# Performance work log

Hardware: AMD Instinct MI355X
Metric: run time of the kernel (lower is better)

## Reference

```python
import jax, jax.numpy as jnp
import numpy as np

B, T, S, U = 256, 64, 16, 4  # batch, channels, yt_img_size, upscale_factor


def setup_inputs() -> dict:
    key = jax.random.key(0)
    k1, k2, k3 = jax.random.split(key, 3)
    x = jax.random.normal(k1, (B, T, S, S), dtype=jnp.float32)
    # Stacked per-pixel Linear weights: (P pixels, out=U*U*T, in=T)
    W = jax.random.normal(k2, (S * S, U * U * T, T), dtype=jnp.float32) * 0.05
    b = jax.random.normal(k3, (S * S, U * U * T), dtype=jnp.float32) * 0.01
    return {"x": x, "W": W, "b": b}


def reference(x, W, b):
    Bn, Tn, Sn, _ = x.shape
    P = Sn * Sn
    Un = int(np.sqrt(W.shape[1] // Tn))  # upscale factor, static
    # Per-pixel grouped GEMM: each spatial location has its own Linear(T -> U*U*T)
    xp = x.reshape(Bn, Tn, P).transpose(2, 0, 1)          # (P, B, T)
    y = jnp.einsum('pbt,pot->pbo', xp, W) + b[:, None, :]  # (P, B, U*U*T)
    # Flat output per pixel is viewed as (T, U, U) and scattered to the (i*U:(i+1)*U, j*U:(j+1)*U) patch
    y = y.reshape(Sn, Sn, Bn, Tn, Un, Un)                  # (Si, Sj, B, T, Ui, Uj)
    y = y.transpose(2, 3, 0, 4, 1, 5)                      # (B, T, Si, Ui, Sj, Uj)
    return y.reshape(Bn, Tn, Sn * Un, Sn * Un)
```

## Files before the change

### kernel.cpp

```cpp
#include <hip/hip_runtime.h>
#include <hip/hip_bf16.h>


#define P_PIX 256
#define BATCH 256
#define KDIM 64
#define ODIM 1024
#define LDA 72

using bf16x8 = __attribute__((ext_vector_type(8))) short;
using f32x4  = __attribute__((ext_vector_type(4))) float;

__global__ __launch_bounds__(256) void transpose_convert(
    const float* __restrict__ x, __hip_bfloat16* __restrict__ xp)
{
    __shared__ float tile[64][65];
    const int R = BATCH * KDIM;
    int p0 = (blockIdx.x & 3) * 64;
    int r0 = (blockIdx.x >> 2) * 64;
    int tp = threadIdx.x & 63;
    int t4 = threadIdx.x >> 6;
    #pragma unroll
    for (int i = 0; i < 16; ++i) {
        int r = t4 + i * 4;
        tile[r][tp] = x[(size_t)(r0 + r) * P_PIX + p0 + tp];
    }
    __syncthreads();
    #pragma unroll
    for (int i = 0; i < 16; ++i) {
        int pl = t4 + i * 4;
        xp[(size_t)(p0 + pl) * R + r0 + tp] = __float2bfloat16(tile[tp][pl]);
    }
}

__global__ __launch_bounds__(256, 2) void gemm_pixel(
    const __hip_bfloat16* __restrict__ xp,
    const float* __restrict__ W,
    const float* __restrict__ bias,
    float* __restrict__ out)
{
    __shared__ __hip_bfloat16 As[128 * LDA];
    __shared__ __hip_bfloat16 Bs[128 * LDA];

    int g = blockIdx.x;
    int nt     = g & 7;
    int sjmod4 = (g >> 3) & 3;
    int q      = g >> 5;
    int mt  = q & 1;
    int sjg = (q >> 1) & 3;
    int si  = q >> 3;
    int p  = si * 16 + sjg * 4 + sjmod4;
    int m0 = mt * 128;
    int n0 = nt * 128;
    int tid = threadIdx.x;

    {
        const uint4* src = (const uint4*)(xp + (size_t)p * (BATCH * KDIM) + (size_t)m0 * KDIM);
        #pragma unroll
        for (int c = 0; c < 4; ++c) {
            int idx = c * 256 + tid;
            int row = idx >> 3, ch = idx & 7;
            uint4 v = src[idx];
            *(uint4*)(&As[row * LDA + ch * 8]) = v;
        }
    }
    {
        const float4* src = (const float4*)(W + (size_t)p * (ODIM * KDIM) + (size_t)n0 * KDIM);
        #pragma unroll
        for (int c = 0; c < 8; ++c) {
            int idx = c * 256 + tid;
            int row = idx >> 4, ch = idx & 15;
            float4 v = src[idx];
            __hip_bfloat16 h[4];
            h[0] = __float2bfloat16(v.x); h[1] = __float2bfloat16(v.y);
            h[2] = __float2bfloat16(v.z); h[3] = __float2bfloat16(v.w);
            *(uint2*)(&Bs[row * LDA + ch * 4]) = *(const uint2*)h;
        }
    }
    __syncthreads();

    int wave = tid >> 6;
    int lane = tid & 63;
    int wm = (wave & 1) * 64;
    int wn = (wave >> 1) * 64;
    int lrow = lane & 15;
    int quad = lane >> 4;

    f32x4 acc[4][4] = {};
    #pragma unroll
    for (int ks = 0; ks < 2; ++ks) {
        bf16x8 a[4], b[4];
        int kof = ks * 32 + quad * 8;
        #pragma unroll
        for (int i = 0; i < 4; ++i)
            a[i] = *(const bf16x8*)(&As[(wm + i * 16 + lrow) * LDA + kof]);
        #pragma unroll
        for (int i = 0; i < 4; ++i)
            b[i] = *(const bf16x8*)(&Bs[(wn + i * 16 + lrow) * LDA + kof]);
        #pragma unroll
        for (int i = 0; i < 4; ++i)
            #pragma unroll
            for (int j = 0; j < 4; ++j)
                acc[i][j] = __builtin_amdgcn_mfma_f32_16x16x32_bf16(a[i], b[j], acc[i][j], 0, 0, 0);
    }

    int sj = p & 15;
    #pragma unroll
    for (int j = 0; j < 4; ++j) {
        int o = n0 + wn + j * 16 + lrow;
        float bv = bias[(size_t)p * ODIM + o];
        int t = o >> 4, ui = (o >> 2) & 3, uj = o & 3;
        size_t base = ((size_t)t * 64 + si * 4 + ui) * 64 + sj * 4 + uj;
        #pragma unroll
        for (int i = 0; i < 4; ++i) {
            int brow = m0 + wm + i * 16 + quad * 4;
            #pragma unroll
            for (int r = 0; r < 4; ++r) {
                out[(size_t)(brow + r) * (64 * 64 * 64) + base] = acc[i][j][r] + bv;
            }
        }
    }
}

extern "C" void kernel_launch(void* const* d_in, const int* in_sizes, int n_in,
                              void* d_out, int out_size, void* d_ws, size_t ws_size,
                              hipStream_t stream) {
    const float* x    = (const float*)d_in[0];
    const float* W    = (const float*)d_in[1];
    const float* bias = (const float*)d_in[2];
    float* out = (float*)d_out;
    __hip_bfloat16* xp = (__hip_bfloat16*)d_ws;

    transpose_convert<<<1024, 256, 0, stream>>>(x, xp);
    gemm_pixel<<<4096, 256, 0, stream>>>(xp, W, bias, out);
}
```

Measured before the change: 478.5 us.

## Restructure per-pixel GEMM to write contiguous output rows without shared memory

Replaces the 128x128 LDS-tiled GEMM with a register-only kernel. Each block covers one output channel t, one pixel row si and 64 batches, and loops over the 16 sj pixels. The MFMA operands are swapped so each lane holds 4 consecutive output elements (ui fixed, uj 0..3), which allows vectorized float4 stores to contiguous output rows instead of scattered scalar stores. W and x are read directly from global memory and converted to bf16 in registers. This removes the LDS traffic and barriers, but W is now reloaded by each of the four batch-tile blocks with no shared reuse.

Result: slower. 572.4 us (+19.6%).

```diff
diff --git a/kernel.cpp b/kernel.cpp
--- a/kernel.cpp
+++ b/kernel.cpp
@@ -6,7 +6,6 @@
 #define BATCH 256
 #define KDIM 64
 #define ODIM 1024
-#define LDA 72
 
 using bf16x8 = __attribute__((ext_vector_type(8))) short;
 using f32x4  = __attribute__((ext_vector_type(4))) float;
@@ -33,91 +32,65 @@
     }
 }
 
-__global__ __launch_bounds__(256, 2) void gemm_pixel(
+__device__ __forceinline__ bf16x8 cvt8(f32x4 a, f32x4 b) {
+    __hip_bfloat16 h[8];
+    h[0] = __float2bfloat16(a[0]); h[1] = __float2bfloat16(a[1]);
+    h[2] = __float2bfloat16(a[2]); h[3] = __float2bfloat16(a[3]);
+    h[4] = __float2bfloat16(b[0]); h[5] = __float2bfloat16(b[1]);
+    h[6] = __float2bfloat16(b[2]); h[7] = __float2bfloat16(b[3]);
+    return *(bf16x8*)h;
+}
+
+__global__ __launch_bounds__(256, 4) void gemm_pixel_t(
     const __hip_bfloat16* __restrict__ xp,
     const float* __restrict__ W,
     const float* __restrict__ bias,
     float* __restrict__ out)
 {
-    __shared__ __hip_bfloat16 As[128 * LDA];
-    __shared__ __hip_bfloat16 Bs[128 * LDA];
+    const int id    = blockIdx.x;
+    const int xcd   = id & 7;
+    const int l     = id >> 3;
+    const int btile = l & 3;
+    const int u     = l >> 2;
+    const int si    = u >> 3;
+    const int t     = (u & 7) * 8 + xcd;
+    const int tid   = threadIdx.x;
+    const int wave  = tid >> 6;
+    const int lane  = tid & 63;
+    const int lrow  = lane & 15;
+    const int quad  = lane >> 4;
+    const int b     = btile * 64 + wave * 16 + lrow;
 
-    int g = blockIdx.x;
-    int nt     = g & 7;
-    int sjmod4 = (g >> 3) & 3;
-    int q      = g >> 5;
-    int mt  = q & 1;
-    int sjg = (q >> 1) & 3;
-    int si  = q >> 3;
-    int p  = si * 16 + sjg * 4 + sjmod4;
-    int m0 = mt * 128;
-    int n0 = nt * 128;
-    int tid = threadIdx.x;
+    const __hip_bfloat16* xr0 = xp + (size_t)(si * 16) * (BATCH * KDIM)
+                                   + (size_t)b * KDIM + quad * 8;
+    const float* wr0 = W + (size_t)(si * 16) * (ODIM * KDIM)
+                         + (size_t)(t * 16 + lrow) * KDIM + quad * 8;
+    const float* br0 = bias + (size_t)(si * 16) * ODIM + t * 16 + quad * 4;
+    float* orow = out + ((size_t)b * 64 + t) * 4096 + (si * 4 + quad) * 64;
 
-    {
-        const uint4* src = (const uint4*)(xp + (size_t)p * (BATCH * KDIM) + (size_t)m0 * KDIM);
+    #pragma unroll
+    for (int g = 0; g < 2; ++g) {
+        f32x4 acc[8];
         #pragma unroll
-        for (int c = 0; c < 4; ++c) {
-            int idx = c * 256 + tid;
-            int row = idx >> 3, ch = idx & 7;
-            uint4 v = src[idx];
-            *(uint4*)(&As[row * LDA + ch * 8]) = v;
+        for (int s = 0; s < 8; ++s) {
+            const int sj = g * 8 + s;
+            const __hip_bfloat16* xr = xr0 + (size_t)sj * (BATCH * KDIM);
+            const float*          wr = wr0 + (size_t)sj * (ODIM * KDIM);
+            bf16x8 xv0 = *(const bf16x8*)(xr);
+            bf16x8 xv1 = *(const bf16x8*)(xr + 32);
+            f32x4 w0 = *(const f32x4*)(wr);
+            f32x4 w1 = *(const f32x4*)(wr + 4);
+            f32x4 w2 = *(const f32x4*)(wr + 32);
+            f32x4 w3 = *(const f32x4*)(wr + 36);
+            f32x4 c = {};
+            c = __builtin_amdgcn_mfma_f32_16x16x32_bf16(cvt8(w0, w1), xv0, c, 0, 0, 0);
+            c = __builtin_amdgcn_mfma_f32_16x16x32_bf16(cvt8(w2, w3), xv1, c, 0, 0, 0);
+            c += *(const f32x4*)(br0 + (size_t)sj * ODIM);
+            acc[s] = c;
         }
-    }
-    {
-        const float4* src = (const float4*)(W + (size_t)p * (ODIM * KDIM) + (size_t)n0 * KDIM);
         #pragma unroll
-        for (int c = 0; c < 8; ++c) {
-            int idx = c * 256 + tid;
-            int row = idx >> 4, ch = idx & 15;
-            float4 v = src[idx];
-            __hip_bfloat16 h[4];
-            h[0] = __float2bfloat16(v.x); h[1] = __float2bfloat16(v.y);
-            h[2] = __float2bfloat16(v.z); h[3] = __float2bfloat16(v.w);
-            *(uint2*)(&Bs[row * LDA + ch * 4]) = *(const uint2*)h;
-        }
-    }
-    __syncthreads();
-
-    int wave = tid >> 6;
-    int lane = tid & 63;
-    int wm = (wave & 1) * 64;
-    int wn = (wave >> 1) * 64;
-    int lrow = lane & 15;
-    int quad = lane >> 4;
-
-    f32x4 acc[4][4] = {};
-    #pragma unroll
-    for (int ks = 0; ks < 2; ++ks) {
-        bf16x8 a[4], b[4];
-        int kof = ks * 32 + quad * 8;
-        #pragma unroll
-        for (int i = 0; i < 4; ++i)
-            a[i] = *(const bf16x8*)(&As[(wm + i * 16 + lrow) * LDA + kof]);
-        #pragma unroll
-        for (int i = 0; i < 4; ++i)
-            b[i] = *(const bf16x8*)(&Bs[(wn + i * 16 + lrow) * LDA + kof]);
-        #pragma unroll
-        for (int i = 0; i < 4; ++i)
-            #pragma unroll
-            for (int j = 0; j < 4; ++j)
-                acc[i][j] = __builtin_amdgcn_mfma_f32_16x16x32_bf16(a[i], b[j], acc[i][j], 0, 0, 0);
-    }
-
-    int sj = p & 15;
-    #pragma unroll
-    for (int j = 0; j < 4; ++j) {
-        int o = n0 + wn + j * 16 + lrow;
-        float bv = bias[(size_t)p * ODIM + o];
-        int t = o >> 4, ui = (o >> 2) & 3, uj = o & 3;
-        size_t base = ((size_t)t * 64 + si * 4 + ui) * 64 + sj * 4 + uj;
-        #pragma unroll
-        for (int i = 0; i < 4; ++i) {
-            int brow = m0 + wm + i * 16 + quad * 4;
-            #pragma unroll
-            for (int r = 0; r < 4; ++r) {
-                out[(size_t)(brow + r) * (64 * 64 * 64) + base] = acc[i][j][r] + bv;
-            }
+        for (int s = 0; s < 8; ++s) {
+            *(f32x4*)(orow + (g * 8 + s) * 4) = acc[s];
         }
     }
 }
@@ -132,5 +105,5 @@
     __hip_bfloat16* xp = (__hip_bfloat16*)d_ws;
 
     transpose_convert<<<1024, 256, 0, stream>>>(x, xp);
-    gemm_pixel<<<4096, 256, 0, stream>>>(xp, W, bias, out);
+    gemm_pixel_t<<<4096, 256, 0, stream>>>(xp, W, bias, out);
 }
```
